# Kernel tuning notes

Hardware: AMD Instinct MI355X
Metric: run time of the kernel (lower is better)

## Reference

```python
import jax, jax.numpy as jnp
import numpy as np

TAU1, TAU2, TSCALE = 30.0, 5.0, 6.0   # tau1 > tau2, in frame units (hz=None)
B, T_OUT = 1000, 20000                # neurons x output frames


def _biexp_kernel():
    # exact replica of SpikeToCalcium.set_double_exp
    r = TAU1 / TAU2
    d = TAU1 - TAU2
    scale = np.power(r, -TAU2 / d) - np.power(r, -TAU1 / d)
    t = np.arange(1.0, TAU1 * TSCALE + 2.0, dtype=np.float32)  # 181 taps
    e1 = np.exp(-t / TAU1)
    e2 = np.exp(-t / TAU2)
    return ((e1 - e2) / scale).astype(np.float32)


def setup_inputs() -> dict:
    key = jax.random.key(0)
    kernel = jnp.asarray(_biexp_kernel())           # (181,)
    Kt = kernel.shape[0]
    u = jax.random.normal(key, (B, T_OUT + Kt - 1), dtype=jnp.float32)  # (1000, 20180)
    return {"u": u, "kernel": kernel}


def reference(u, kernel):
    # Original: K.conv1d(u[..., None], kernel[::-1, None, None], 1, 'valid')
    # keras conv1d is cross-correlation; reversing the kernel makes it a true
    # causal FIR convolution. lax.conv_general_dilated is also cross-correlation,
    # so we pass the reversed kernel identically.
    rhs = kernel[::-1][None, None, :]               # (O=1, I=1, K)
    lhs = u[:, None, :]                             # (B, C=1, T_in)
    out = jax.lax.conv_general_dilated(
        lhs, rhs, window_strides=(1,), padding='VALID',
        dimension_numbers=('NCH', 'OIH', 'NCH'))
    return out[:, 0, :]                             # (B, T_in - K + 1)
```

## Files before the change

### kernel.cpp

```cpp
#include <hip/hip_runtime.h>

namespace {
constexpr int kB   = 1000;
constexpr int kT   = 20000;
constexpr int kKt  = 181;
constexpr int kInW = kT + kKt - 1;
constexpr int BM   = 16;
constexpr int BT   = 512;
constexpr int NCHUNK = 7;
constexpr int COLS = (BT - 16) + NCHUNK * 32;
constexpr int LDS_STRIDE = COLS + 8;

typedef short bf16x8 __attribute__((ext_vector_type(8)));
typedef float f32x4  __attribute__((ext_vector_type(4)));

__device__ __forceinline__ short f32_bf16(float f) {
  union { float f; unsigned u; } x; x.f = f;
  unsigned r = x.u + (0x7fffu + ((x.u >> 16) & 1u));
  return (short)(r >> 16);
}
}

__global__ __launch_bounds__(256, 4)
void biexp_conv_mfma(const float* __restrict__ u, const float* __restrict__ kern,
                     float* __restrict__ out) {
  __shared__ short lds_u[BM * LDS_STRIDE];
  __shared__ float lds_k[kKt];

  const int tid  = threadIdx.x;
  const int lane = tid & 63;
  const int wave = tid >> 6;
  const int quad = lane >> 4;
  const int nn   = lane & 15;
  const int b0 = blockIdx.y * BM;
  const int t0 = blockIdx.x * BT;

  if (tid < kKt) lds_k[tid] = kern[tid];

  const int nvec = (COLS / 4) * BM;
  for (int f = tid; f < nvec; f += 256) {
    int r  = f / (COLS / 4);
    int c4 = f - r * (COLS / 4);
    int row = b0 + r; row = row < kB ? row : kB - 1;
    int col = t0 + c4 * 4;
    const float* src = u + (size_t)row * kInW;
    float v0, v1, v2, v3;
    if (col + 3 < kInW) {
      float4 v = *(const float4*)(src + col);
      v0 = v.x; v1 = v.y; v2 = v.z; v3 = v.w;
    } else {
      int cm = kInW - 1;
      v0 = src[col     < cm ? col     : cm];
      v1 = src[col + 1 < cm ? col + 1 : cm];
      v2 = src[col + 2 < cm ? col + 2 : cm];
      v3 = src[col + 3 < cm ? col + 3 : cm];
    }
    short4 s;
    s.x = f32_bf16(v0); s.y = f32_bf16(v1); s.z = f32_bf16(v2); s.w = f32_bf16(v3);
    *(short4*)(&lds_u[r * LDS_STRIDE + c4 * 4]) = s;
  }
  __syncthreads();

  bf16x8 bfrag[NCHUNK];
  #pragma unroll
  for (int c = 0; c < NCHUNK; ++c) {
    #pragma unroll
    for (int j = 0; j < 8; ++j) {
      int idx = 32 * c + quad * 8 + j - nn;
      float v = (idx >= 0 && idx < kKt) ? lds_k[kKt - 1 - idx] : 0.0f;
      bfrag[c][j] = f32_bf16(v);
    }
  }

  const short* arow = &lds_u[nn * LDS_STRIDE + quad * 8];
  #pragma unroll 2
  for (int jt = 0; jt < BT / 64; ++jt) {
    const int nt = wave * (BT / 4) + jt * 16;
    f32x4 acc = {0.f, 0.f, 0.f, 0.f};
    #pragma unroll
    for (int c = 0; c < NCHUNK; ++c) {
      bf16x8 a = *(const bf16x8*)(arow + nt + 32 * c);
      acc = __builtin_amdgcn_mfma_f32_16x16x32_bf16(a, bfrag[c], acc, 0, 0, 0);
    }
    const int gt = t0 + nt + nn;
    #pragma unroll
    for (int r = 0; r < 4; ++r) {
      const int gb = b0 + quad * 4 + r;
      if (gb < kB && gt < kT) out[(size_t)gb * kT + gt] = acc[r];
    }
  }
}

extern "C" void kernel_launch(void* const* d_in, const int* in_sizes, int n_in,
                              void* d_out, int out_size, void* d_ws, size_t ws_size,
                              hipStream_t stream) {
  const float* u  = (const float*)d_in[0];
  const float* kn = (const float*)d_in[1];
  float* out = (float*)d_out;
  dim3 grid((kT + BT - 1) / BT, (kB + BM - 1) / BM);
  hipLaunchKernelGGL(biexp_conv_mfma, grid, dim3(256, 1, 1), 0, stream, u, kn, out);
}
```

Baseline: 158.2 us.

## Add unrolled interior tile load path, nontemporal stores, raise occupancy hint

Adds a fast path for interior tiles: the halo width is rounded up to 768 columns and each thread issues 12 independent float4 loads before converting them to bf16 and writing them to LDS. This removes per-element division, clamping and bounds branches, and puts more memory requests in flight. Edge tiles keep the old generic loop. Output writes now use nontemporal stores, and the launch-bounds occupancy hint rises from 4 to 6. The trade-offs are extra over-fetch and LDS per block, plus added register pressure.

```diff
diff --git a/kernel.cpp b/kernel.cpp
--- a/kernel.cpp
+++ b/kernel.cpp
@@ -8,7 +8,8 @@
 constexpr int BM   = 16;
 constexpr int BT   = 512;
 constexpr int NCHUNK = 7;
-constexpr int COLS = (BT - 16) + NCHUNK * 32;
+constexpr int NEED = (BT - 16) + NCHUNK * 32;
+constexpr int COLS = 768;
 constexpr int LDS_STRIDE = COLS + 8;
 
 typedef short bf16x8 __attribute__((ext_vector_type(8)));
@@ -21,7 +22,7 @@
 }
 }
 
-__global__ __launch_bounds__(256, 4)
+__global__ __launch_bounds__(256, 6)
 void biexp_conv_mfma(const float* __restrict__ u, const float* __restrict__ kern,
                      float* __restrict__ out) {
   __shared__ short lds_u[BM * LDS_STRIDE];
@@ -37,27 +38,44 @@
 
   if (tid < kKt) lds_k[tid] = kern[tid];
 
-  const int nvec = (COLS / 4) * BM;
-  for (int f = tid; f < nvec; f += 256) {
-    int r  = f / (COLS / 4);
-    int c4 = f - r * (COLS / 4);
-    int row = b0 + r; row = row < kB ? row : kB - 1;
-    int col = t0 + c4 * 4;
-    const float* src = u + (size_t)row * kInW;
-    float v0, v1, v2, v3;
-    if (col + 3 < kInW) {
-      float4 v = *(const float4*)(src + col);
-      v0 = v.x; v1 = v.y; v2 = v.z; v3 = v.w;
-    } else {
-      int cm = kInW - 1;
-      v0 = src[col     < cm ? col     : cm];
-      v1 = src[col + 1 < cm ? col + 1 : cm];
-      v2 = src[col + 2 < cm ? col + 2 : cm];
-      v3 = src[col + 3 < cm ? col + 3 : cm];
+  const bool interior = (t0 + COLS <= kInW) && (b0 + BM <= kB);
+  if (interior) {
+    const int r  = tid >> 4;
+    const int c0 = tid & 15;
+    const float* src = u + (size_t)(b0 + r) * kInW + t0 + c0 * 4;
+    short* dst = &lds_u[r * LDS_STRIDE + c0 * 4];
+    float4 v[12];
+    #pragma unroll
+    for (int i = 0; i < 12; ++i) v[i] = *(const float4*)(src + i * 64);
+    #pragma unroll
+    for (int i = 0; i < 12; ++i) {
+      short4 s;
+      s.x = f32_bf16(v[i].x); s.y = f32_bf16(v[i].y);
+      s.z = f32_bf16(v[i].z); s.w = f32_bf16(v[i].w);
+      *(short4*)(dst + i * 64) = s;
     }
-    short4 s;
-    s.x = f32_bf16(v0); s.y = f32_bf16(v1); s.z = f32_bf16(v2); s.w = f32_bf16(v3);
-    *(short4*)(&lds_u[r * LDS_STRIDE + c4 * 4]) = s;
+  } else {
+    for (int f = tid; f < (NEED / 4) * BM; f += 256) {
+      int r  = f / (NEED / 4);
+      int c4 = f - r * (NEED / 4);
+      int row = b0 + r; row = row < kB ? row : kB - 1;
+      int col = t0 + c4 * 4;
+      const float* src = u + (size_t)row * kInW;
+      float v0, v1, v2, v3;
+      if (col + 3 < kInW) {
+        float4 v = *(const float4*)(src + col);
+        v0 = v.x; v1 = v.y; v2 = v.z; v3 = v.w;
+      } else {
+        int cm = kInW - 1;
+        v0 = src[col     < cm ? col     : cm];
+        v1 = src[col + 1 < cm ? col + 1 : cm];
+        v2 = src[col + 2 < cm ? col + 2 : cm];
+        v3 = src[col + 3 < cm ? col + 3 : cm];
+      }
+      short4 s;
+      s.x = f32_bf16(v0); s.y = f32_bf16(v1); s.z = f32_bf16(v2); s.w = f32_bf16(v3);
+      *(short4*)(&lds_u[r * LDS_STRIDE + c4 * 4]) = s;
+    }
   }
   __syncthreads();
 
@@ -86,7 +104,8 @@
     #pragma unroll
     for (int r = 0; r < 4; ++r) {
       const int gb = b0 + quad * 4 + r;
-      if (gb < kB && gt < kT) out[(size_t)gb * kT + gt] = acc[r];
+      if (gb < kB && gt < kT)
+        __builtin_nontemporal_store(acc[r], &out[(size_t)gb * kT + gt]);
     }
   }
 }
```

Result: no change. 159.1 us (+0.6%).

## Stream input fragments directly from global into registers, dropping LDS staging

Applied to the files above, without the earlier changes.

Each wave now independently handles a 16-row by 128-column job. It loads the input straight from global memory into bf16 MFMA A-fragments held in registers and reuses them across output tiles through a sliding window, instead of staging a block tile in shared memory. The two interleaved accumulators cut the MFMA dependency chain, and the tail case is handled through a compile-time specialisation. This removes the LDS round trip and the block-wide barrier. In exchange, neighbouring waves reload overlapping halo data from global memory and each thread uses more registers.

```diff
diff --git a/kernel.cpp b/kernel.cpp
--- a/kernel.cpp
+++ b/kernel.cpp
@@ -1,94 +1,120 @@
 #include <hip/hip_runtime.h>
+#include <hip/hip_bf16.h>
 
 namespace {
 constexpr int kB   = 1000;
 constexpr int kT   = 20000;
 constexpr int kKt  = 181;
 constexpr int kInW = kT + kKt - 1;
-constexpr int BM   = 16;
-constexpr int BT   = 512;
-constexpr int NCHUNK = 7;
-constexpr int COLS = (BT - 16) + NCHUNK * 32;
-constexpr int LDS_STRIDE = COLS + 8;
+constexpr int TW     = 128;
+constexpr int NTILE  = TW / 16;
+constexpr int NFRAG  = NTILE + 12;
+constexpr int NB     = (kB + 15) / 16;
+constexpr int NS     = (kT + TW - 1) / TW;
+constexpr int NJOBS  = NB * NS;
+constexpr int WPB    = 4;
+constexpr int NBLK   = (NJOBS + WPB - 1) / WPB;
 
 typedef short bf16x8 __attribute__((ext_vector_type(8)));
 typedef float f32x4  __attribute__((ext_vector_type(4)));
 
-__device__ __forceinline__ short f32_bf16(float f) {
-  union { float f; unsigned u; } x; x.f = f;
-  unsigned r = x.u + (0x7fffu + ((x.u >> 16) & 1u));
-  return (short)(r >> 16);
-}
+__device__ __forceinline__ unsigned pack_bf16x2(float lo, float hi) {
+  __hip_bfloat162 h = __float22bfloat162_rn(float2{lo, hi});
+  unsigned w;
+  __builtin_memcpy(&w, &h, 4);
+  return w;
 }
 
-__global__ __launch_bounds__(256, 4)
-void biexp_conv_mfma(const float* __restrict__ u, const float* __restrict__ kern,
-                     float* __restrict__ out) {
-  __shared__ short lds_u[BM * LDS_STRIDE];
+template <bool B> struct TailTag { static constexpr bool value = B; };
+}
+
+__global__ __launch_bounds__(256, 3)
+void biexp_stream(const float* __restrict__ u, const float* __restrict__ kern,
+                  float* __restrict__ out) {
   __shared__ float lds_k[kKt];
+  const int tid = threadIdx.x;
+  if (tid < kKt) lds_k[tid] = kern[tid];
+  __syncthreads();
 
-  const int tid  = threadIdx.x;
   const int lane = tid & 63;
   const int wave = tid >> 6;
   const int quad = lane >> 4;
   const int nn   = lane & 15;
-  const int b0 = blockIdx.y * BM;
-  const int t0 = blockIdx.x * BT;
 
-  if (tid < kKt) lds_k[tid] = kern[tid];
-
-  const int nvec = (COLS / 4) * BM;
-  for (int f = tid; f < nvec; f += 256) {
-    int r  = f / (COLS / 4);
-    int c4 = f - r * (COLS / 4);
-    int row = b0 + r; row = row < kB ? row : kB - 1;
-    int col = t0 + c4 * 4;
-    const float* src = u + (size_t)row * kInW;
-    float v0, v1, v2, v3;
-    if (col + 3 < kInW) {
-      float4 v = *(const float4*)(src + col);
-      v0 = v.x; v1 = v.y; v2 = v.z; v3 = v.w;
-    } else {
-      int cm = kInW - 1;
-      v0 = src[col     < cm ? col     : cm];
-      v1 = src[col + 1 < cm ? col + 1 : cm];
-      v2 = src[col + 2 < cm ? col + 2 : cm];
-      v3 = src[col + 3 < cm ? col + 3 : cm];
-    }
-    short4 s;
-    s.x = f32_bf16(v0); s.y = f32_bf16(v1); s.z = f32_bf16(v2); s.w = f32_bf16(v3);
-    *(short4*)(&lds_u[r * LDS_STRIDE + c4 * 4]) = s;
-  }
-  __syncthreads();
-
-  bf16x8 bfrag[NCHUNK];
+  union { bf16x8 v; unsigned w[4]; } bfr[7];
   #pragma unroll
-  for (int c = 0; c < NCHUNK; ++c) {
+  for (int c = 0; c < 7; ++c) {
     #pragma unroll
-    for (int j = 0; j < 8; ++j) {
-      int idx = 32 * c + quad * 8 + j - nn;
-      float v = (idx >= 0 && idx < kKt) ? lds_k[kKt - 1 - idx] : 0.0f;
-      bfrag[c][j] = f32_bf16(v);
+    for (int jj = 0; jj < 4; ++jj) {
+      int i0 = 32 * c + quad * 8 + 2 * jj - nn;
+      float f0 = (i0 >= 0     && i0 < kKt)     ? lds_k[kKt - 1 - i0] : 0.0f;
+      float f1 = (i0 + 1 >= 0 && i0 + 1 < kKt) ? lds_k[kKt - 2 - i0] : 0.0f;
+      bfr[c].w[jj] = pack_bf16x2(f0, f1);
     }
   }
 
-  const short* arow = &lds_u[nn * LDS_STRIDE + quad * 8];
-  #pragma unroll 2
-  for (int jt = 0; jt < BT / 64; ++jt) {
-    const int nt = wave * (BT / 4) + jt * 16;
-    f32x4 acc = {0.f, 0.f, 0.f, 0.f};
+  const int job = blockIdx.x * WPB + wave;
+  if (job >= NJOBS) return;
+  const int jb = job / NS;
+  const int js = job - jb * NS;
+  const int b0 = jb * 16;
+  const int t0 = js * TW;
+
+  const int row = min(b0 + nn, kB - 1);
+  const float* __restrict__ urow = u + (size_t)row * kInW;
+
+  auto body = [&](auto tail_tag) {
+    constexpr bool TAIL = decltype(tail_tag)::value;
+    auto load_frag = [&](int m) -> bf16x8 {
+      int col = t0 + 16 * m + quad * 8;
+      union { bf16x8 v; unsigned w[4]; } r;
+      if (!TAIL || col + 8 <= kInW) {
+        f32x4 a = *(const f32x4*)(urow + col);
+        f32x4 b = *(const f32x4*)(urow + col + 4);
+        r.w[0] = pack_bf16x2(a[0], a[1]);
+        r.w[1] = pack_bf16x2(a[2], a[3]);
+        r.w[2] = pack_bf16x2(b[0], b[1]);
+        r.w[3] = pack_bf16x2(b[2], b[3]);
+      } else {
+        float e[8];
+        #pragma unroll
+        for (int j = 0; j < 8; ++j) e[j] = urow[min(col + j, kInW - 1)];
+        r.w[0] = pack_bf16x2(e[0], e[1]);
+        r.w[1] = pack_bf16x2(e[2], e[3]);
+        r.w[2] = pack_bf16x2(e[4], e[5]);
+        r.w[3] = pack_bf16x2(e[6], e[7]);
+      }
+      return r.v;
+    };
+
+    bf16x8 F[NFRAG];
     #pragma unroll
-    for (int c = 0; c < NCHUNK; ++c) {
-      bf16x8 a = *(const bf16x8*)(arow + nt + 32 * c);
-      acc = __builtin_amdgcn_mfma_f32_16x16x32_bf16(a, bfrag[c], acc, 0, 0, 0);
+    for (int m = 0; m < 14; ++m) F[m] = load_frag(m);
+
+    #pragma unroll
+    for (int jt = 0; jt < NTILE; ++jt) {
+      if (jt + 14 < NFRAG) F[jt + 14] = load_frag(jt + 14);
+      f32x4 acc0 = {0.f, 0.f, 0.f, 0.f};
+      f32x4 acc1 = {0.f, 0.f, 0.f, 0.f};
+      #pragma unroll
+      for (int c = 0; c < 7; c += 2)
+        acc0 = __builtin_amdgcn_mfma_f32_16x16x32_bf16(F[jt + 2 * c], bfr[c].v, acc0, 0, 0, 0);
+      #pragma unroll
+      for (int c = 1; c < 7; c += 2)
+        acc1 = __builtin_amdgcn_mfma_f32_16x16x32_bf16(F[jt + 2 * c], bfr[c].v, acc1, 0, 0, 0);
+      const int gt = t0 + 16 * jt + nn;
+      if (gt < kT) {
+        #pragma unroll
+        for (int r = 0; r < 4; ++r) {
+          const int gb = b0 + quad * 4 + r;
+          if (gb < kB) out[(size_t)gb * kT + gt] = acc0[r] + acc1[r];
+        }
+      }
     }
-    const int gt = t0 + nt + nn;
-    #pragma unroll
-    for (int r = 0; r < 4; ++r) {
-      const int gb = b0 + quad * 4 + r;
-      if (gb < kB && gt < kT) out[(size_t)gb * kT + gt] = acc[r];
-    }
-  }
+  };
+
+  if (js == NS - 1) body(TailTag<true>{});
+  else              body(TailTag<false>{});
 }
 
 extern "C" void kernel_launch(void* const* d_in, const int* in_sizes, int n_in,
@@ -97,6 +123,6 @@
   const float* u  = (const float*)d_in[0];
   const float* kn = (const float*)d_in[1];
   float* out = (float*)d_out;
-  dim3 grid((kT + BT - 1) / BT, (kB + BM - 1) / BM);
-  hipLaunchKernelGGL(biexp_conv_mfma, grid, dim3(256, 1, 1), 0, stream, u, kn, out);
+  hipLaunchKernelGGL(biexp_stream, dim3(NBLK, 1, 1), dim3(256, 1, 1), 0, stream,
+                     u, kn, out);
 }
```

Result: slower. 162.9 us (+3.0%).
